# Optimization experiments

Measured on AMD Instinct MI355X. Metric: run time of the kernel, lower is better.

## Reference

```python
import jax, jax.numpy as jnp
import numpy as np

BETA = 0.9
TH = 1.0  # snn.Leaky default threshold
SPARSITY = 0.5


@jax.custom_vjp
def spike(x):
    # Heaviside spike; surrogate (atan, alpha=2) gradient as in snntorch default
    return (x > 0).astype(x.dtype)

def _spike_fwd(x):
    return spike(x), x

def _spike_bwd(x, g):
    return (g / (1.0 + (jnp.pi * x) ** 2),)

spike.defvjp(_spike_fwd, _spike_bwd)


def setup_inputs() -> dict:
    key = jax.random.key(0)
    ks = jax.random.split(key, 6)
    T, B, NIN, NH, NOUT = 50, 512, 784, 1000, 10

    def mk_w(k, o, i):
        k1, k2 = jax.random.split(k)
        w = jax.random.normal(k1, (o, i), jnp.float32) * (1.0 / np.sqrt(i))
        mask = (jax.random.uniform(k2, (o, i)) > SPARSITY).astype(jnp.float32)
        return w * mask

    x = jax.random.normal(ks[0], (T, B, NIN), jnp.float32)
    return dict(
        x=x,
        W0=mk_w(ks[1], NH, NIN), b0=jnp.zeros((NH,), jnp.float32),
        W1=mk_w(ks[2], NH, NH), b1=jnp.zeros((NH,), jnp.float32),
        W2=mk_w(ks[3], NH, NH), b2=jnp.zeros((NH,), jnp.float32),
        W3=mk_w(ks[4], NOUT, NH), b3=jnp.zeros((NOUT,), jnp.float32),
    )


def reference(x, W0, b0, W1, b1, W2, b2, W3, b3):
    params = ((W0, b0), (W1, b1), (W2, b2), (W3, b3))
    B = x.shape[1]
    mems0 = tuple(jnp.zeros((B, W.shape[0]), x.dtype) for W, _ in params)

    def step(mems, xt):
        inp = xt
        new_mems, spks = [], []
        for (W, b), m in zip(params, mems):
            cur = inp @ W.T + b
            # snntorch Leaky (reset_mechanism='subtract'):
            # reset from previous mem (detached), then mem = beta*mem + I - reset*th
            reset = jax.lax.stop_gradient((m > TH).astype(x.dtype))
            m_new = BETA * m + cur - reset * TH
            s = spike(m_new - TH)
            new_mems.append(m_new)
            spks.append(s)
            inp = s
        return tuple(new_mems), (tuple(spks), tuple(new_mems))

    _, (spk_rec, mem_rec) = jax.lax.scan(step, mems0, x)
    # spk_rec/mem_rec: tuples of [T, B, dim] arrays per layer
    return (*spk_rec, *mem_rec)
```

## Files before the change

kernel.cpp:

```cpp
#include <hip/hip_runtime.h>


typedef int int4v  __attribute__((ext_vector_type(4)));
typedef int int16v __attribute__((ext_vector_type(16)));

#define XSCALE 68719476736.0
#define WSCALE 1099511627776.0
#define MT 25600

__global__ void wsplit_i8(const float* __restrict__ W, signed char* __restrict__ out,
                          int Nreal, int Npad, int K, int Kpad)
{
    int idx = blockIdx.x * blockDim.x + threadIdx.x;
    int total = Npad * Kpad;
    if (idx >= total) return;
    int n = idx / Kpad, k = idx - n * Kpad;
    long long v = 0;
    if (n < Nreal && k < K) v = __double2ll_rn((double)W[(size_t)n * K + k] * WSCALE);
    size_t plane = (size_t)total;
#pragma unroll
    for (int p = 0; p < 4; ++p) {
        int d = (int)(v & 255); if (d > 127) d -= 256;
        out[p * plane + idx] = (signed char)d;
        v = (v - d) >> 8;
    }
    out[4 * plane + idx] = (signed char)v;
}

__global__ void wsplit_i8x2(const float* __restrict__ Wa, signed char* __restrict__ oa,
                            const float* __restrict__ Wb, signed char* __restrict__ ob)
{
    const float* W = blockIdx.y ? Wb : Wa;
    signed char* out = blockIdx.y ? ob : oa;
    int idx = blockIdx.x * blockDim.x + threadIdx.x;
    const int total = 1024 * 1024;
    if (idx >= total) return;
    int n = idx >> 10, k = idx & 1023;
    long long v = 0;
    if (n < 1000 && k < 1000) v = __double2ll_rn((double)W[(size_t)n * 1000 + k] * WSCALE);
    size_t plane = (size_t)total;
#pragma unroll
    for (int p = 0; p < 4; ++p) {
        int d = (int)(v & 255); if (d > 127) d -= 256;
        out[p * plane + idx] = (signed char)d;
        v = (v - d) >> 8;
    }
    out[4 * plane + idx] = (signed char)v;
}

__device__ __forceinline__ void digit16(const float* __restrict__ xr, int k0,
                                        int4v (&D)[5])
{
    float xv[16];
    if (k0 + 16 <= 784) {
#pragma unroll
        for (int q = 0; q < 4; ++q) {
            float4 f = *(const float4*)(xr + k0 + q * 4);
            xv[q * 4 + 0] = f.x; xv[q * 4 + 1] = f.y;
            xv[q * 4 + 2] = f.z; xv[q * 4 + 3] = f.w;
        }
    } else {
#pragma unroll
        for (int j = 0; j < 16; ++j) xv[j] = 0.f;
    }
    unsigned pk[5][4];
#pragma unroll
    for (int p = 0; p < 5; ++p)
#pragma unroll
        for (int q = 0; q < 4; ++q) pk[p][q] = 0;
#pragma unroll
    for (int j = 0; j < 16; ++j) {
        long long v = __double2ll_rn((double)xv[j] * XSCALE);
#pragma unroll
        for (int p = 0; p < 4; ++p) {
            int d = (int)(v & 255); if (d > 127) d -= 256;
            pk[p][j >> 2] |= (unsigned)(d & 255) << ((j & 3) * 8);
            v = (v - d) >> 8;
        }
        pk[4][j >> 2] |= (unsigned)((int)v & 255) << ((j & 3) * 8);
    }
#pragma unroll
    for (int p = 0; p < 5; ++p)
        D[p] = (int4v){(int)pk[p][0], (int)pk[p][1], (int)pk[p][2], (int)pk[p][3]};
}

__global__ __launch_bounds__(256)
void gemm32_l0(const float* __restrict__ x,
               const signed char* __restrict__ Wp, size_t planeW,
               double* __restrict__ curout)
{
    constexpr int KP = 832, NIT = 13;
    __shared__ __align__(16) signed char Wld[5 * 64 * 80];
    __shared__ __align__(16) signed char Ald[5 * 64 * 80];

    const int tid = threadIdx.x;
    const int l   = tid & 63;
    const int w   = tid >> 6;
    const int wm  = (w & 1) * 32;
    const int wn  = (w >> 1) * 32;
    const int r32 = l & 31;
    const int h   = l >> 5;

    const int bm = blockIdx.y * 64;
    const int bn = blockIdx.x * 64;

    const int srow = tid >> 2;
    const int sc   = (tid & 3) * 16;

    const float* xr = x + (size_t)(bm + srow) * 784;
    const signed char* wg = Wp + (size_t)(bn + srow) * KP + sc;

    int4v Dr[5], Wr[5];
#pragma unroll
    for (int p = 0; p < 5; ++p) Wr[p] = *(const int4v*)(wg + p * planeW);
    digit16(xr, sc, Dr);

    int16v acc[5];
#pragma unroll
    for (int s = 0; s < 5; ++s)
#pragma unroll
        for (int r = 0; r < 16; ++r) acc[s][r] = 0;

    for (int it = 0; it < NIT; ++it) {
        __syncthreads();
#pragma unroll
        for (int p = 0; p < 5; ++p) {
            *(int4v*)&Wld[(p * 64 + srow) * 80 + sc] = Wr[p];
            *(int4v*)&Ald[(p * 64 + srow) * 80 + sc] = Dr[p];
        }
        __syncthreads();

        if (it + 1 < NIT) {
            int kb = (it + 1) * 64;
#pragma unroll
            for (int p = 0; p < 5; ++p)
                Wr[p] = *(const int4v*)(wg + kb + p * planeW);
            digit16(xr, kb + sc, Dr);
        }

#pragma unroll
        for (int k2 = 0; k2 < 2; ++k2) {
            const int off = k2 * 32 + 16 * h;
            int4v af[5], bq[5];
#pragma unroll
            for (int p = 0; p < 5; ++p)
                af[p] = *(const int4v*)&Ald[(p * 64 + wm + r32) * 80 + off];
#pragma unroll
            for (int q = 0; q < 5; ++q)
                bq[q] = *(const int4v*)&Wld[(q * 64 + wn + r32) * 80 + off];
#pragma unroll
            for (int q = 0; q < 5; ++q)
#pragma unroll
                for (int p = 0; p < 5; ++p)
                    if (p + q >= 4)
                        acc[p + q - 4] = __builtin_amdgcn_mfma_i32_32x32x32_i8(
                            af[p], bq[q], acc[p + q - 4], 0, 0, 0);
        }
    }

    const int col = bn + wn + r32;
#pragma unroll
    for (int reg = 0; reg < 16; ++reg) {
        int row = bm + wm + (reg & 3) + 8 * (reg >> 2) + 4 * h;
        double v = (double)acc[4][reg];
        v = v * 256.0 + (double)acc[3][reg];
        v = v * 256.0 + (double)acc[2][reg];
        v = v * 256.0 + (double)acc[1][reg];
        v = v * 256.0 + (double)acc[0][reg];
        curout[(size_t)row * 1024 + col] = v * 0x1p-44;
    }
}

template<int KP, int CS>
__global__ __launch_bounds__(256)
void gemm32(const signed char* __restrict__ Ap,
            const signed char* __restrict__ Wp, size_t planeW,
            double* __restrict__ curout)
{
    __shared__ __align__(16) signed char Wld[5 * 64 * 80];
    __shared__ __align__(16) signed char Ald[64 * 80];
    constexpr int NIT = KP / 64;

    const int tid = threadIdx.x;
    const int l   = tid & 63;
    const int w   = tid >> 6;
    const int wm  = (w & 1) * 32;
    const int wn  = (w >> 1) * 32;
    const int r32 = l & 31;
    const int h   = l >> 5;

    const int bm = blockIdx.y * 64;
    const int bn = blockIdx.x * 64;

    const int srow = tid >> 2;
    const int sc   = (tid & 3) * 16;

    const signed char* ag = Ap + (size_t)(bm + srow) * KP + sc;
    const signed char* wg = Wp + (size_t)(bn + srow) * KP + sc;

    int4v Ar, Wr[5];
#pragma unroll
    for (int p = 0; p < 5; ++p) Wr[p] = *(const int4v*)(wg + p * planeW);
    Ar = *(const int4v*)ag;

    int16v acc[5];
#pragma unroll
    for (int s = 0; s < 5; ++s)
#pragma unroll
        for (int r = 0; r < 16; ++r) acc[s][r] = 0;

    for (int it = 0; it < NIT; ++it) {
        __syncthreads();
#pragma unroll
        for (int p = 0; p < 5; ++p)
            *(int4v*)&Wld[(p * 64 + srow) * 80 + sc] = Wr[p];
        *(int4v*)&Ald[srow * 80 + sc] = Ar;
        __syncthreads();

        if (it + 1 < NIT) {
            int kb = (it + 1) * 64;
#pragma unroll
            for (int p = 0; p < 5; ++p)
                Wr[p] = *(const int4v*)(wg + kb + p * planeW);
            Ar = *(const int4v*)(ag + kb);
        }

#pragma unroll
        for (int k2 = 0; k2 < 2; ++k2) {
            const int off = k2 * 32 + 16 * h;
            int4v a0 = *(const int4v*)&Ald[(wm + r32) * 80 + off];
#pragma unroll
            for (int q = 0; q < 5; ++q) {
                int4v bq = *(const int4v*)&Wld[(q * 64 + wn + r32) * 80 + off];
                acc[q] = __builtin_amdgcn_mfma_i32_32x32x32_i8(a0, bq, acc[q], 0, 0, 0);
            }
        }
    }

    const int col = bn + wn + r32;
    if (col < CS) {
#pragma unroll
        for (int reg = 0; reg < 16; ++reg) {
            int row = bm + wm + (reg & 3) + 8 * (reg >> 2) + 4 * h;
            double v = (double)acc[4][reg];
            v = v * 256.0 + (double)acc[3][reg];
            v = v * 256.0 + (double)acc[2][reg];
            v = v * 256.0 + (double)acc[1][reg];
            v = v * 256.0 + (double)acc[0][reg];
            curout[(size_t)row * CS + col] = v * 0x1p-40;
        }
    }
}

template<int KP>
__global__ __launch_bounds__(256)
void gemm32w(const signed char* __restrict__ Asp,
             const signed char* __restrict__ Wp, size_t planeW,
             double* __restrict__ curout)
{
    __shared__ __align__(16) signed char Wld[5 * 64 * 80];
    __shared__ __align__(16) signed char Ald[128 * 80];
    constexpr int NIT = KP / 64;

    const int tid = threadIdx.x;
    const int l   = tid & 63;
    const int w   = tid >> 6;
    const int wm  = (w & 1) * 64;
    const int wn  = (w >> 1) * 32;
    const int r32 = l & 31;
    const int h   = l >> 5;

    const int bm = blockIdx.y * 128;
    const int bn = blockIdx.x * 64;

    const int srA = tid >> 1;
    const int scA = (tid & 1) * 32;
    const int srW = tid >> 2;
    const int scW = (tid & 3) * 16;

    const signed char* ag = Asp + (size_t)(bm + srA) * KP + scA;
    const signed char* wg = Wp  + (size_t)(bn + srW) * KP + scW;

    int4v Ar0 = *(const int4v*)(ag);
    int4v Ar1 = *(const int4v*)(ag + 16);
    int4v Wr[5];
#pragma unroll
    for (int p = 0; p < 5; ++p) Wr[p] = *(const int4v*)(wg + p * planeW);

    int16v acc[2][5];
#pragma unroll
    for (int mi = 0; mi < 2; ++mi)
#pragma unroll
        for (int s = 0; s < 5; ++s)
#pragma unroll
            for (int r = 0; r < 16; ++r) acc[mi][s][r] = 0;

    for (int it = 0; it < NIT; ++it) {
        __syncthreads();
#pragma unroll
        for (int p = 0; p < 5; ++p)
            *(int4v*)&Wld[(p * 64 + srW) * 80 + scW] = Wr[p];
        *(int4v*)&Ald[srA * 80 + scA]      = Ar0;
        *(int4v*)&Ald[srA * 80 + scA + 16] = Ar1;
        __syncthreads();

        if (it + 1 < NIT) {
            int kb = (it + 1) * 64;
            Ar0 = *(const int4v*)(ag + kb);
            Ar1 = *(const int4v*)(ag + kb + 16);
#pragma unroll
            for (int p = 0; p < 5; ++p)
                Wr[p] = *(const int4v*)(wg + kb + p * planeW);
        }

#pragma unroll
        for (int k2 = 0; k2 < 2; ++k2) {
            const int off = k2 * 32 + 16 * h;
            int4v bq[5];
#pragma unroll
            for (int q = 0; q < 5; ++q)
                bq[q] = *(const int4v*)&Wld[(q * 64 + wn + r32) * 80 + off];
#pragma unroll
            for (int mi = 0; mi < 2; ++mi) {
                int4v a0 = *(const int4v*)&Ald[(wm + mi * 32 + r32) * 80 + off];
#pragma unroll
                for (int q = 0; q < 5; ++q)
                    acc[mi][q] = __builtin_amdgcn_mfma_i32_32x32x32_i8(
                        a0, bq[q], acc[mi][q], 0, 0, 0);
            }
        }
    }

    const int col = bn + wn + r32;
#pragma unroll
    for (int mi = 0; mi < 2; ++mi)
#pragma unroll
        for (int reg = 0; reg < 16; ++reg) {
            int row = bm + wm + mi * 32 + (reg & 3) + 8 * (reg >> 2) + 4 * h;
            double v = (double)acc[mi][4][reg];
            v = v * 256.0 + (double)acc[mi][3][reg];
            v = v * 256.0 + (double)acc[mi][2][reg];
            v = v * 256.0 + (double)acc[mi][1][reg];
            v = v * 256.0 + (double)acc[mi][0][reg];
            curout[(size_t)row * 1024 + col] = v * 0x1p-40;
        }
}

__global__ __launch_bounds__(256)
void if_update(const double* __restrict__ cur, const float* __restrict__ bias,
               float* __restrict__ spk, float* __restrict__ mem,
               signed char* __restrict__ spk_i8)
{
    int idx = blockIdx.x * blockDim.x + threadIdx.x;
    if (idx >= 512 * 512) return;
    int row = idx >> 9, col = (idx & 511) * 2;
    if (col >= 1000) {
        for (int t = 0; t < 50; ++t)
            *(short*)&spk_i8[((size_t)t * 512 + row) * 1024 + col] = 0;
        return;
    }
    double mp0 = 0.0, mp1 = 0.0;
    double bs0 = (double)bias[col], bs1 = (double)bias[col + 1];
    for (int t = 0; t < 50; ++t) {
        double2 c = *(const double2*)&cur[((size_t)t * 512 + row) * 1024 + col];
        double rst0 = (mp0 > 1.0) ? 1.0 : 0.0;
        double rst1 = (mp1 > 1.0) ? 1.0 : 0.0;
        double mn0 = 0.9 * mp0 + (c.x + bs0) - rst0;
        double mn1 = 0.9 * mp1 + (c.y + bs1) - rst1;
        int s0 = (mn0 > 1.0) ? 1 : 0;
        int s1 = (mn1 > 1.0) ? 1 : 0;
        size_t o = ((size_t)t * 512 + row) * 1000 + col;
        *(float2*)&spk[o] = make_float2((float)s0, (float)s1);
        *(float2*)&mem[o] = make_float2((float)mn0, (float)mn1);
        *(short*)&spk_i8[((size_t)t * 512 + row) * 1024 + col] =
            (short)(s0 | (s1 << 8));
        mp0 = mn0; mp1 = mn1;
    }
}

__global__ __launch_bounds__(256)
void if3_kernel(const double* __restrict__ cur3, const float* __restrict__ bias,
                float* __restrict__ spk3, float* __restrict__ mem3)
{
    int idx = blockIdx.x * blockDim.x + threadIdx.x;
    if (idx >= 5120) return;
    int brow = idx / 10, col = idx - brow * 10;
    double bs = (double)bias[col];
    double mp = 0.0;
    for (int t = 0; t < 50; ++t) {
        double c   = cur3[((size_t)t * 512 + brow) * 16 + col] + bs;
        double rst = (mp > 1.0) ? 1.0 : 0.0;
        double mn  = 0.9 * mp + c - rst;
        size_t o   = (size_t)t * 5120 + (size_t)brow * 10 + col;
        spk3[o] = (mn > 1.0) ? 1.0f : 0.0f;
        mem3[o] = (float)mn;
        mp = mn;
    }
}

extern "C" void kernel_launch(void* const* d_in, const int* in_sizes, int n_in,
                              void* d_out, int out_size, void* d_ws, size_t ws_size,
                              hipStream_t stream)
{
    const float* x  = (const float*)d_in[0];
    const float* W0 = (const float*)d_in[1];
    const float* b0 = (const float*)d_in[2];
    const float* W1 = (const float*)d_in[3];
    const float* b1 = (const float*)d_in[4];
    const float* W2 = (const float*)d_in[5];
    const float* b2 = (const float*)d_in[6];
    const float* W3 = (const float*)d_in[7];
    const float* b3 = (const float*)d_in[8];
    float* out = (float*)d_out;

    const int T = 50;
    const size_t LNH = (size_t)512 * 1000;
    const size_t LNO = (size_t)512 * 10;

    float* spk0 = out;
    float* spk1 = spk0 + (size_t)T * LNH;
    float* spk2 = spk1 + (size_t)T * LNH;
    float* spk3 = spk2 + (size_t)T * LNH;
    float* mem0 = spk3 + (size_t)T * LNO;
    float* mem1 = mem0 + (size_t)T * LNH;
    float* mem2 = mem1 + (size_t)T * LNH;
    float* mem3 = mem2 + (size_t)T * LNH;

    double* cur = (double*)d_ws;
    signed char* W0d = (signed char*)(cur + (size_t)MT * 1024);
    signed char* W1d = W0d + (size_t)5 * 1024 * 832;
    signed char* W2d = W1d + (size_t)5 * 1024 * 1024;
    signed char* W3d = W2d + (size_t)5 * 1024 * 1024;
    signed char* sp0 = W3d + (size_t)5 * 64 * 1024;
    signed char* sp1 = sp0 + (size_t)MT * 1024;
    signed char* sp2 = sp1 + (size_t)MT * 1024;

    wsplit_i8<<<(1024 * 832 + 255) / 256, 256, 0, stream>>>(W0, W0d, 1000, 1024, 784, 832);
    wsplit_i8x2<<<dim3((1024 * 1024 + 255) / 256, 2), 256, 0, stream>>>(W1, W1d, W2, W2d);
    wsplit_i8<<<(64 * 1024 + 255) / 256, 256, 0, stream>>>(W3, W3d, 10, 64, 1000, 1024);

    const size_t plW0 = (size_t)1024 * 832;
    const size_t plWH = (size_t)1024 * 1024;
    const size_t plW3 = (size_t)64 * 1024;

    dim3 blk(256);
    dim3 g0(16, MT / 64);
    dim3 gW(16, MT / 128);
    dim3 g3(1, MT / 64);

    gemm32_l0<<<g0, blk, 0, stream>>>(x, W0d, plW0, cur);
    if_update<<<1024, 256, 0, stream>>>(cur, b0, spk0, mem0, sp0);
    gemm32w<1024><<<gW, blk, 0, stream>>>(sp0, W1d, plWH, cur);
    if_update<<<1024, 256, 0, stream>>>(cur, b1, spk1, mem1, sp1);
    gemm32w<1024><<<gW, blk, 0, stream>>>(sp1, W2d, plWH, cur);
    if_update<<<1024, 256, 0, stream>>>(cur, b2, spk2, mem2, sp2);
    gemm32<1024, 16><<<g3, blk, 0, stream>>>(sp2, W3d, plW3, cur);
    if3_kernel<<<20, 256, 0, stream>>>(cur, b3, spk3, mem3);
}
```

Before: 1.206 ms.

## Pre-split input digits once and load A fragments directly from global memory

The on-the-fly splitting of x into five int8 digit planes inside the layer-0 GEMM moves into a separate xsplit_all pass, so 16 column blocks no longer repeat that double-precision digit work. Both the layer-0 and hidden-layer GEMMs now read A operand fragments straight from global memory into registers and drop the A LDS staging plus its stores. The layer-3 GEMM becomes a dedicated non-template kernel. The costs are an extra pass that writes and then re-reads about 100MB of digit planes, and A loads that are less coalesced because they come from strided global rows.

```diff
diff --git a/kernel.cpp b/kernel.cpp
--- a/kernel.cpp
+++ b/kernel.cpp
@@ -48,50 +48,31 @@
     out[4 * plane + idx] = (signed char)v;
 }
 
-__device__ __forceinline__ void digit16(const float* __restrict__ xr, int k0,
-                                        int4v (&D)[5])
-{
-    float xv[16];
-    if (k0 + 16 <= 784) {
-#pragma unroll
-        for (int q = 0; q < 4; ++q) {
-            float4 f = *(const float4*)(xr + k0 + q * 4);
-            xv[q * 4 + 0] = f.x; xv[q * 4 + 1] = f.y;
-            xv[q * 4 + 2] = f.z; xv[q * 4 + 3] = f.w;
-        }
-    } else {
-#pragma unroll
-        for (int j = 0; j < 16; ++j) xv[j] = 0.f;
-    }
-    unsigned pk[5][4];
-#pragma unroll
-    for (int p = 0; p < 5; ++p)
-#pragma unroll
-        for (int q = 0; q < 4; ++q) pk[p][q] = 0;
-#pragma unroll
-    for (int j = 0; j < 16; ++j) {
-        long long v = __double2ll_rn((double)xv[j] * XSCALE);
-#pragma unroll
-        for (int p = 0; p < 4; ++p) {
-            int d = (int)(v & 255); if (d > 127) d -= 256;
-            pk[p][j >> 2] |= (unsigned)(d & 255) << ((j & 3) * 8);
-            v = (v - d) >> 8;
-        }
-        pk[4][j >> 2] |= (unsigned)((int)v & 255) << ((j & 3) * 8);
-    }
-#pragma unroll
-    for (int p = 0; p < 5; ++p)
-        D[p] = (int4v){(int)pk[p][0], (int)pk[p][1], (int)pk[p][2], (int)pk[p][3]};
+__global__ void xsplit_all(const float* __restrict__ x, signed char* __restrict__ out)
+{
+    int idx = blockIdx.x * blockDim.x + threadIdx.x;
+    if (idx >= MT * 832) return;
+    int row = idx / 832, k = idx - row * 832;
+    long long v = 0;
+    if (k < 784) v = __double2ll_rn((double)x[(size_t)row * 784 + k] * XSCALE);
+    const size_t plane = (size_t)MT * 832;
+    signed char* o = out + idx;
+#pragma unroll
+    for (int p = 0; p < 4; ++p) {
+        int d = (int)(v & 255); if (d > 127) d -= 256;
+        o[p * plane] = (signed char)d;
+        v = (v - d) >> 8;
+    }
+    o[4 * plane] = (signed char)v;
 }
 
 __global__ __launch_bounds__(256)
-void gemm32_l0(const float* __restrict__ x,
-               const signed char* __restrict__ Wp, size_t planeW,
-               double* __restrict__ curout)
+void gemm_l0g(const signed char* __restrict__ Ap, size_t planeA,
+              const signed char* __restrict__ Wp, size_t planeW,
+              double* __restrict__ curout)
 {
     constexpr int KP = 832, NIT = 13;
     __shared__ __align__(16) signed char Wld[5 * 64 * 80];
-    __shared__ __align__(16) signed char Ald[5 * 64 * 80];
 
     const int tid = threadIdx.x;
     const int l   = tid & 63;
@@ -107,13 +88,12 @@
     const int srow = tid >> 2;
     const int sc   = (tid & 3) * 16;
 
-    const float* xr = x + (size_t)(bm + srow) * 784;
-    const signed char* wg = Wp + (size_t)(bn + srow) * KP + sc;
-
-    int4v Dr[5], Wr[5];
+    const signed char* wg  = Wp + (size_t)(bn + srow) * KP + sc;
+    const signed char* agf = Ap + (size_t)(bm + wm + r32) * KP + 16 * h;
+
+    int4v Wr[5];
 #pragma unroll
     for (int p = 0; p < 5; ++p) Wr[p] = *(const int4v*)(wg + p * planeW);
-    digit16(xr, sc, Dr);
 
     int16v acc[5];
 #pragma unroll
@@ -122,29 +102,30 @@
         for (int r = 0; r < 16; ++r) acc[s][r] = 0;
 
     for (int it = 0; it < NIT; ++it) {
-        __syncthreads();
+        const int kb = it * 64;
+        __syncthreads();
+#pragma unroll
+        for (int p = 0; p < 5; ++p)
+            *(int4v*)&Wld[(p * 64 + srow) * 80 + sc] = Wr[p];
+        __syncthreads();
+
+        if (it + 1 < NIT) {
+#pragma unroll
+            for (int p = 0; p < 5; ++p)
+                Wr[p] = *(const int4v*)(wg + kb + 64 + p * planeW);
+        }
+
+        int4v afl[5], afh[5];
 #pragma unroll
         for (int p = 0; p < 5; ++p) {
-            *(int4v*)&Wld[(p * 64 + srow) * 80 + sc] = Wr[p];
-            *(int4v*)&Ald[(p * 64 + srow) * 80 + sc] = Dr[p];
-        }
-        __syncthreads();
-
-        if (it + 1 < NIT) {
-            int kb = (it + 1) * 64;
-#pragma unroll
-            for (int p = 0; p < 5; ++p)
-                Wr[p] = *(const int4v*)(wg + kb + p * planeW);
-            digit16(xr, kb + sc, Dr);
+            afl[p] = *(const int4v*)(agf + p * planeA + kb);
+            afh[p] = *(const int4v*)(agf + p * planeA + kb + 32);
         }
 
 #pragma unroll
         for (int k2 = 0; k2 < 2; ++k2) {
             const int off = k2 * 32 + 16 * h;
-            int4v af[5], bq[5];
-#pragma unroll
-            for (int p = 0; p < 5; ++p)
-                af[p] = *(const int4v*)&Ald[(p * 64 + wm + r32) * 80 + off];
+            int4v bq[5];
 #pragma unroll
             for (int q = 0; q < 5; ++q)
                 bq[q] = *(const int4v*)&Wld[(q * 64 + wn + r32) * 80 + off];
@@ -154,7 +135,7 @@
                 for (int p = 0; p < 5; ++p)
                     if (p + q >= 4)
                         acc[p + q - 4] = __builtin_amdgcn_mfma_i32_32x32x32_i8(
-                            af[p], bq[q], acc[p + q - 4], 0, 0, 0);
+                            k2 ? afh[p] : afl[p], bq[q], acc[p + q - 4], 0, 0, 0);
         }
     }
 
@@ -171,96 +152,14 @@
     }
 }
 
-template<int KP, int CS>
-__global__ __launch_bounds__(256)
-void gemm32(const signed char* __restrict__ Ap,
-            const signed char* __restrict__ Wp, size_t planeW,
-            double* __restrict__ curout)
-{
-    __shared__ __align__(16) signed char Wld[5 * 64 * 80];
-    __shared__ __align__(16) signed char Ald[64 * 80];
-    constexpr int NIT = KP / 64;
-
-    const int tid = threadIdx.x;
-    const int l   = tid & 63;
-    const int w   = tid >> 6;
-    const int wm  = (w & 1) * 32;
-    const int wn  = (w >> 1) * 32;
-    const int r32 = l & 31;
-    const int h   = l >> 5;
-
-    const int bm = blockIdx.y * 64;
-    const int bn = blockIdx.x * 64;
-
-    const int srow = tid >> 2;
-    const int sc   = (tid & 3) * 16;
-
-    const signed char* ag = Ap + (size_t)(bm + srow) * KP + sc;
-    const signed char* wg = Wp + (size_t)(bn + srow) * KP + sc;
-
-    int4v Ar, Wr[5];
-#pragma unroll
-    for (int p = 0; p < 5; ++p) Wr[p] = *(const int4v*)(wg + p * planeW);
-    Ar = *(const int4v*)ag;
-
-    int16v acc[5];
-#pragma unroll
-    for (int s = 0; s < 5; ++s)
-#pragma unroll
-        for (int r = 0; r < 16; ++r) acc[s][r] = 0;
-
-    for (int it = 0; it < NIT; ++it) {
-        __syncthreads();
-#pragma unroll
-        for (int p = 0; p < 5; ++p)
-            *(int4v*)&Wld[(p * 64 + srow) * 80 + sc] = Wr[p];
-        *(int4v*)&Ald[srow * 80 + sc] = Ar;
-        __syncthreads();
-
-        if (it + 1 < NIT) {
-            int kb = (it + 1) * 64;
-#pragma unroll
-            for (int p = 0; p < 5; ++p)
-                Wr[p] = *(const int4v*)(wg + kb + p * planeW);
-            Ar = *(const int4v*)(ag + kb);
-        }
-
-#pragma unroll
-        for (int k2 = 0; k2 < 2; ++k2) {
-            const int off = k2 * 32 + 16 * h;
-            int4v a0 = *(const int4v*)&Ald[(wm + r32) * 80 + off];
-#pragma unroll
-            for (int q = 0; q < 5; ++q) {
-                int4v bq = *(const int4v*)&Wld[(q * 64 + wn + r32) * 80 + off];
-                acc[q] = __builtin_amdgcn_mfma_i32_32x32x32_i8(a0, bq, acc[q], 0, 0, 0);
-            }
-        }
-    }
-
-    const int col = bn + wn + r32;
-    if (col < CS) {
-#pragma unroll
-        for (int reg = 0; reg < 16; ++reg) {
-            int row = bm + wm + (reg & 3) + 8 * (reg >> 2) + 4 * h;
-            double v = (double)acc[4][reg];
-            v = v * 256.0 + (double)acc[3][reg];
-            v = v * 256.0 + (double)acc[2][reg];
-            v = v * 256.0 + (double)acc[1][reg];
-            v = v * 256.0 + (double)acc[0][reg];
-            curout[(size_t)row * CS + col] = v * 0x1p-40;
-        }
-    }
-}
-
 template<int KP>
 __global__ __launch_bounds__(256)
-void gemm32w(const signed char* __restrict__ Asp,
-             const signed char* __restrict__ Wp, size_t planeW,
-             double* __restrict__ curout)
-{
+void gemm_spg(const signed char* __restrict__ Asp,
+              const signed char* __restrict__ Wp, size_t planeW,
+              double* __restrict__ curout)
+{
+    constexpr int NIT = KP / 64;
     __shared__ __align__(16) signed char Wld[5 * 64 * 80];
-    __shared__ __align__(16) signed char Ald[128 * 80];
-    constexpr int NIT = KP / 64;
 
     const int tid = threadIdx.x;
     const int l   = tid & 63;
@@ -273,19 +172,20 @@
     const int bm = blockIdx.y * 128;
     const int bn = blockIdx.x * 64;
 
-    const int srA = tid >> 1;
-    const int scA = (tid & 1) * 32;
     const int srW = tid >> 2;
     const int scW = (tid & 3) * 16;
 
-    const signed char* ag = Asp + (size_t)(bm + srA) * KP + scA;
-    const signed char* wg = Wp  + (size_t)(bn + srW) * KP + scW;
-
-    int4v Ar0 = *(const int4v*)(ag);
-    int4v Ar1 = *(const int4v*)(ag + 16);
+    const signed char* wg  = Wp + (size_t)(bn + srW) * KP + scW;
+    const signed char* ag0 = Asp + (size_t)(bm + wm + r32) * KP + 16 * h;
+    const signed char* ag1 = Asp + (size_t)(bm + wm + 32 + r32) * KP + 16 * h;
+
     int4v Wr[5];
 #pragma unroll
     for (int p = 0; p < 5; ++p) Wr[p] = *(const int4v*)(wg + p * planeW);
+    int4v al0 = *(const int4v*)(ag0);
+    int4v ah0 = *(const int4v*)(ag0 + 32);
+    int4v al1 = *(const int4v*)(ag1);
+    int4v ah1 = *(const int4v*)(ag1 + 32);
 
     int16v acc[2][5];
 #pragma unroll
@@ -300,17 +200,19 @@
 #pragma unroll
         for (int p = 0; p < 5; ++p)
             *(int4v*)&Wld[(p * 64 + srW) * 80 + scW] = Wr[p];
-        *(int4v*)&Ald[srA * 80 + scA]      = Ar0;
-        *(int4v*)&Ald[srA * 80 + scA + 16] = Ar1;
-        __syncthreads();
-
-        if (it + 1 < NIT) {
-            int kb = (it + 1) * 64;
-            Ar0 = *(const int4v*)(ag + kb);
-            Ar1 = *(const int4v*)(ag + kb + 16);
+        __syncthreads();
+
+        int4v nl0, nh0, nl1, nh1;
+        const bool more = (it + 1 < NIT);
+        if (more) {
+            int kb2 = (it + 1) * 64;
 #pragma unroll
             for (int p = 0; p < 5; ++p)
-                Wr[p] = *(const int4v*)(wg + kb + p * planeW);
+                Wr[p] = *(const int4v*)(wg + kb2 + p * planeW);
+            nl0 = *(const int4v*)(ag0 + kb2);
+            nh0 = *(const int4v*)(ag0 + kb2 + 32);
+            nl1 = *(const int4v*)(ag1 + kb2);
+            nh1 = *(const int4v*)(ag1 + kb2 + 32);
         }
 
 #pragma unroll
@@ -320,15 +222,15 @@
 #pragma unroll
             for (int q = 0; q < 5; ++q)
                 bq[q] = *(const int4v*)&Wld[(q * 64 + wn + r32) * 80 + off];
-#pragma unroll
-            for (int mi = 0; mi < 2; ++mi) {
-                int4v a0 = *(const int4v*)&Ald[(wm + mi * 32 + r32) * 80 + off];
-#pragma unroll
-                for (int q = 0; q < 5; ++q)
-                    acc[mi][q] = __builtin_amdgcn_mfma_i32_32x32x32_i8(
-                        a0, bq[q], acc[mi][q], 0, 0, 0);
+            int4v a0 = k2 ? ah0 : al0;
+            int4v a1 = k2 ? ah1 : al1;
+#pragma unroll
+            for (int q = 0; q < 5; ++q) {
+                acc[0][q] = __builtin_amdgcn_mfma_i32_32x32x32_i8(a0, bq[q], acc[0][q], 0, 0, 0);
+                acc[1][q] = __builtin_amdgcn_mfma_i32_32x32x32_i8(a1, bq[q], acc[1][q], 0, 0, 0);
             }
         }
+        if (more) { al0 = nl0; ah0 = nh0; al1 = nl1; ah1 = nh1; }
     }
 
     const int col = bn + wn + r32;
@@ -344,6 +246,86 @@
             v = v * 256.0 + (double)acc[mi][0][reg];
             curout[(size_t)row * 1024 + col] = v * 0x1p-40;
         }
+}
+
+__global__ __launch_bounds__(256)
+void gemm32_l3(const signed char* __restrict__ Ap,
+               const signed char* __restrict__ Wp, size_t planeW,
+               double* __restrict__ curout)
+{
+    constexpr int KP = 1024, NIT = 16;
+    __shared__ __align__(16) signed char Wld[5 * 64 * 80];
+    __shared__ __align__(16) signed char Ald[64 * 80];
+
+    const int tid = threadIdx.x;
+    const int l   = tid & 63;
+    const int w   = tid >> 6;
+    const int wm  = (w & 1) * 32;
+    const int wn  = (w >> 1) * 32;
+    const int r32 = l & 31;
+    const int h   = l >> 5;
+
+    const int bm = blockIdx.y * 64;
+    const int bn = 0;
+
+    const int srow = tid >> 2;
+    const int sc   = (tid & 3) * 16;
+
+    const signed char* ag = Ap + (size_t)(bm + srow) * KP + sc;
+    const signed char* wg = Wp + (size_t)(bn + srow) * KP + sc;
+
+    int4v Ar, Wr[5];
+#pragma unroll
+    for (int p = 0; p < 5; ++p) Wr[p] = *(const int4v*)(wg + p * planeW);
+    Ar = *(const int4v*)ag;
+
+    int16v acc[5];
+#pragma unroll
+    for (int s = 0; s < 5; ++s)
+#pragma unroll
+        for (int r = 0; r < 16; ++r) acc[s][r] = 0;
+
+    for (int it = 0; it < NIT; ++it) {
+        __syncthreads();
+#pragma unroll
+        for (int p = 0; p < 5; ++p)
+            *(int4v*)&Wld[(p * 64 + srow) * 80 + sc] = Wr[p];
+        *(int4v*)&Ald[srow * 80 + sc] = Ar;
+        __syncthreads();
+
+        if (it + 1 < NIT) {
+            int kb = (it + 1) * 64;
+#pragma unroll
+            for (int p = 0; p < 5; ++p)
+                Wr[p] = *(const int4v*)(wg + kb + p * planeW);
+            Ar = *(const int4v*)(ag + kb);
+        }
+
+#pragma unroll
+        for (int k2 = 0; k2 < 2; ++k2) {
+            const int off = k2 * 32 + 16 * h;
+            int4v a0 = *(const int4v*)&Ald[(wm + r32) * 80 + off];
+#pragma unroll
+            for (int q = 0; q < 5; ++q) {
+                int4v bq = *(const int4v*)&Wld[(q * 64 + wn + r32) * 80 + off];
+                acc[q] = __builtin_amdgcn_mfma_i32_32x32x32_i8(a0, bq, acc[q], 0, 0, 0);
+            }
+        }
+    }
+
+    const int col = bn + wn + r32;
+    if (col < 16) {
+#pragma unroll
+        for (int reg = 0; reg < 16; ++reg) {
+            int row = bm + wm + (reg & 3) + 8 * (reg >> 2) + 4 * h;
+            double v = (double)acc[4][reg];
+            v = v * 256.0 + (double)acc[3][reg];
+            v = v * 256.0 + (double)acc[2][reg];
+            v = v * 256.0 + (double)acc[1][reg];
+            v = v * 256.0 + (double)acc[0][reg];
+            curout[(size_t)row * 16 + col] = v * 0x1p-40;
+        }
+    }
 }
 
 __global__ __launch_bounds__(256)
@@ -431,7 +413,8 @@
     signed char* W1d = W0d + (size_t)5 * 1024 * 832;
     signed char* W2d = W1d + (size_t)5 * 1024 * 1024;
     signed char* W3d = W2d + (size_t)5 * 1024 * 1024;
-    signed char* sp0 = W3d + (size_t)5 * 64 * 1024;
+    signed char* xsb = W3d + (size_t)5 * 64 * 1024;
+    signed char* sp0 = xsb + (size_t)5 * MT * 832;
     signed char* sp1 = sp0 + (size_t)MT * 1024;
     signed char* sp2 = sp1 + (size_t)MT * 1024;
 
@@ -439,6 +422,9 @@
     wsplit_i8x2<<<dim3((1024 * 1024 + 255) / 256, 2), 256, 0, stream>>>(W1, W1d, W2, W2d);
     wsplit_i8<<<(64 * 1024 + 255) / 256, 256, 0, stream>>>(W3, W3d, 10, 64, 1000, 1024);
 
+    xsplit_all<<<(MT * 832 + 255) / 256, 256, 0, stream>>>(x, xsb);
+
+    const size_t plA0 = (size_t)MT * 832;
     const size_t plW0 = (size_t)1024 * 832;
     const size_t plWH = (size_t)1024 * 1024;
     const size_t plW3 = (size_t)64 * 1024;
@@ -448,12 +434,12 @@
     dim3 gW(16, MT / 128);
     dim3 g3(1, MT / 64);
 
-    gemm32_l0<<<g0, blk, 0, stream>>>(x, W0d, plW0, cur);
+    gemm_l0g<<<g0, blk, 0, stream>>>(xsb, plA0, W0d, plW0, cur);
     if_update<<<1024, 256, 0, stream>>>(cur, b0, spk0, mem0, sp0);
-    gemm32w<1024><<<gW, blk, 0, stream>>>(sp0, W1d, plWH, cur);
+    gemm_spg<1024><<<gW, blk, 0, stream>>>(sp0, W1d, plWH, cur);
     if_update<<<1024, 256, 0, stream>>>(cur, b1, spk1, mem1, sp1);
-    gemm32w<1024><<<gW, blk, 0, stream>>>(sp1, W2d, plWH, cur);
+    gemm_spg<1024><<<gW, blk, 0, stream>>>(sp1, W2d, plWH, cur);
     if_update<<<1024, 256, 0, stream>>>(cur, b2, spk2, mem2, sp2);
-    gemm32<1024, 16><<<g3, blk, 0, stream>>>(sp2, W3d, plW3, cur);
+    gemm32_l3<<<g3, blk, 0, stream>>>(sp2, W3d, plW3, cur);
     if3_kernel<<<20, 256, 0, stream>>>(cur, b3, spk3, mem3);
 }
```

Result: no change. 1.194 ms (-1.0%).
